# Performance work log

Measured on AMD Instinct MI355X. Metric: run time of the kernel, lower is better.

Reference implementation:

```python
import jax, jax.numpy as jnp
import numpy as np


def setup_inputs() -> dict:
    key = jax.random.key(0)
    ks = jax.random.split(key, 5)
    B, DEC, ENC, H = 4, 256, 256, 512  # feature_dim = hl_size = 512, mlp hidden = 512
    decoder_states = jax.random.normal(ks[0], (B, DEC, H), dtype=jnp.float32)
    encoder_states = jax.random.normal(ks[1], (B, ENC, H), dtype=jnp.float32)
    ext_mask = jnp.zeros((B, DEC, ENC), dtype=bool)  # self.mask set externally; all-False here
    W_mlp = jax.random.normal(ks[2], (2 * H, H), dtype=jnp.float32) * 0.02  # Linear(2H -> H)
    b_mlp = jnp.zeros((H,), dtype=jnp.float32)
    W_out = jax.random.normal(ks[3], (H, 1), dtype=jnp.float32) * 0.02  # Linear(H -> 1)
    b_out = jnp.zeros((1,), dtype=jnp.float32)
    return {"decoder_states": decoder_states, "encoder_states": encoder_states,
            "ext_mask": ext_mask, "W_mlp": W_mlp, "b_mlp": b_mlp,
            "W_out": W_out, "b_out": b_out}


def reference(decoder_states, encoder_states, ext_mask, W_mlp, b_mlp, W_out, b_out):
    # decoder_states: [B, dec, H]; encoder_states: [B, enc, H]
    H = encoder_states.shape[-1]
    # pad mask: positions where encoder feature-0 equals 0.0 -> [B, 1, enc]
    pad_mask = (encoder_states == 0.0)[:, :, :1]
    pad_mask = jnp.swapaxes(pad_mask, 1, 2)  # [B, 1, enc]
    # cat(enc, dec) @ W_mlp  ==  enc @ W_mlp[:H] + dec @ W_mlp[H:]  (avoids 2H concat)
    enc_proj = jnp.einsum('beh,hm->bem', encoder_states, W_mlp[:H])   # [B, enc, Hm]
    dec_proj = jnp.einsum('bdh,hm->bdm', decoder_states, W_mlp[H:])   # [B, dec, Hm]
    hidden = jnp.tanh(dec_proj[:, :, None, :] + enc_proj[:, None, :, :] + b_mlp)  # [B, dec, enc, Hm]
    attn = jnp.einsum('bdem,mo->bde', hidden, W_out) + b_out[0]       # [B, dec, enc]
    attn = jnp.where(ext_mask, -jnp.inf, attn)
    attn = jnp.where(pad_mask, -jnp.inf, attn)
    attn = jax.nn.softmax(attn, axis=-1)
    context = jnp.einsum('bde,beh->bdh', attn, encoder_states)        # [B, dec, H]
    return (context, attn)
```

## Files before the change

### kernel.cpp

```cpp
#include <hip/hip_runtime.h>
#include <math.h>

#define B 4
#define DEC 256
#define ENC 256
#define HDIM 512

#define TANH_SCALE 2.8853900817779268f
#define LOG2E 1.4426950408889634f

__device__ __forceinline__ float fast_exp2(float x) { return __builtin_amdgcn_exp2f(x); }
__device__ __forceinline__ float fast_rcp(float x)  { return __builtin_amdgcn_rcpf(x); }

typedef __attribute__((ext_vector_type(8))) short bf16x8;
typedef __attribute__((ext_vector_type(4))) short bf16x4;
typedef __attribute__((ext_vector_type(4))) float f32x4;
typedef __attribute__((ext_vector_type(4))) unsigned int u32x4;

__device__ __forceinline__ unsigned short bf16_rne(float x) {
    unsigned u = __float_as_uint(x);
    return (unsigned short)((u + 0x7FFFu + ((u >> 16) & 1u)) >> 16);
}
__device__ __forceinline__ float bf16_to_f(unsigned short h) {
    return __uint_as_float((unsigned)h << 16);
}

#define W_OFS(m, k) ((((long)(m) >> 4) << 13) + (((long)(k) >> 3) << 7) + (((m) & 15) << 3) + ((k) & 7))

__global__ __launch_bounds__(256) void convert_kernel(
    const float* __restrict__ enc, const float* __restrict__ dec,
    const float* __restrict__ Wmlp,
    unsigned short* __restrict__ Xh_e, unsigned short* __restrict__ Xl_e,
    unsigned short* __restrict__ Xh_d, unsigned short* __restrict__ Xl_d,
    unsigned short* __restrict__ Wh_e, unsigned short* __restrict__ Wl_e,
    unsigned short* __restrict__ Wh_d, unsigned short* __restrict__ Wl_d,
    unsigned char* __restrict__ padm)
{
    const int tid = threadIdx.x, z = blockIdx.z;
    if (z < 2) {
        const float* X = z ? dec : enc;
        unsigned short* H = z ? Xh_d : Xh_e;
        unsigned short* L = z ? Xl_d : Xl_e;
        const long i8 = ((long)blockIdx.x * 256 + tid) * 8;
        float4 v0 = *(const float4*)(X + i8);
        float4 v1 = *(const float4*)(X + i8 + 4);
        if (z == 0 && (i8 & 511) == 0)
            padm[i8 >> 9] = (v0.x == 0.0f) ? 1 : 0;
        float xs[8] = {v0.x, v0.y, v0.z, v0.w, v1.x, v1.y, v1.z, v1.w};
        bf16x8 hv, lv;
#pragma unroll
        for (int j = 0; j < 8; ++j) {
            unsigned short h = bf16_rne(xs[j]);
            hv[j] = (short)h;
            lv[j] = (short)bf16_rne(xs[j] - bf16_to_f(h));
        }
        *(bf16x8*)(H + i8) = hv;
        *(bf16x8*)(L + i8) = lv;
    } else {
        const float* Wsrc = Wmlp + (z == 3 ? (long)HDIM * HDIM : 0);
        unsigned short* H = (z == 3) ? Wh_d : Wh_e;
        unsigned short* L = (z == 3) ? Wl_d : Wl_e;
        const int t = blockIdx.x * 256 + tid;
        const int m = t & 511;
        const int k0 = (t >> 9) << 2;
        bf16x4 hv, lv;
#pragma unroll
        for (int j = 0; j < 4; ++j) {
            float x = Wsrc[(long)(k0 + j) * 512 + m];
            unsigned short h = bf16_rne(x);
            hv[j] = (short)h;
            lv[j] = (short)bf16_rne(x - bf16_to_f(h));
        }
        const long ofs = W_OFS(m, k0);
        *(bf16x4*)(H + ofs) = hv;
        *(bf16x4*)(L + ofs) = lv;
    }
}

__global__ __launch_bounds__(256) void proj_mfma_kernel(
    const unsigned short* __restrict__ Xh_e, const unsigned short* __restrict__ Xl_e,
    const unsigned short* __restrict__ Xh_d, const unsigned short* __restrict__ Xl_d,
    const unsigned short* __restrict__ Wh_e, const unsigned short* __restrict__ Wl_e,
    const unsigned short* __restrict__ Wh_d, const unsigned short* __restrict__ Wl_d,
    const float* __restrict__ bmlp,
    unsigned int* __restrict__ ET2, float* __restrict__ Dmat)
{
    const int tid = threadIdx.x;
    const int wave = tid >> 6, lane = tid & 63;
    const int z = blockIdx.z;
    const int r0w = blockIdx.x * 64 + wave * 16;
    const int m0 = blockIdx.y * 32;
    const unsigned short* Xh = z ? Xh_d : Xh_e;
    const unsigned short* Xl = z ? Xl_d : Xl_e;
    const unsigned short* Wh = z ? Wh_d : Wh_e;
    const unsigned short* Wl = z ? Wl_d : Wl_e;

    const int col = lane & 15;
    const int quad = lane >> 4;

    const unsigned short* pah = Xh + (long)(r0w + col) * 512 + quad * 8;
    const unsigned short* pal = Xl + (long)(r0w + col) * 512 + quad * 8;
    const long bofs = ((long)(m0 >> 4) << 13) + (quad << 7) + (col << 3);
    const unsigned short* pb0h = Wh + bofs;
    const unsigned short* pb0l = Wl + bofs;
    const unsigned short* pb1h = Wh + bofs + 8192;
    const unsigned short* pb1l = Wl + bofs + 8192;

    f32x4 a0h = {0.f,0.f,0.f,0.f}, a0x = {0.f,0.f,0.f,0.f};
    f32x4 a1h = {0.f,0.f,0.f,0.f}, a1x = {0.f,0.f,0.f,0.f};

    bf16x8 Ah = *(const bf16x8*)pah,  Al = *(const bf16x8*)pal;
    bf16x8 B0h = *(const bf16x8*)pb0h, B0l = *(const bf16x8*)pb0l;
    bf16x8 B1h = *(const bf16x8*)pb1h, B1l = *(const bf16x8*)pb1l;

#pragma unroll 1
    for (int k0 = 0; k0 < 512; k0 += 32) {
        bf16x8 nAh = Ah, nAl = Al, nB0h = B0h, nB0l = B0l, nB1h = B1h, nB1l = B1l;
        if (k0 + 32 < 512) {
            nAh = *(const bf16x8*)(pah + k0 + 32);
            nAl = *(const bf16x8*)(pal + k0 + 32);
            const long ko = (long)(k0 + 32) << 4;
            nB0h = *(const bf16x8*)(pb0h + ko);
            nB0l = *(const bf16x8*)(pb0l + ko);
            nB1h = *(const bf16x8*)(pb1h + ko);
            nB1l = *(const bf16x8*)(pb1l + ko);
        }
        a0h = __builtin_amdgcn_mfma_f32_16x16x32_bf16(Ah, B0h, a0h, 0, 0, 0);
        a1h = __builtin_amdgcn_mfma_f32_16x16x32_bf16(Ah, B1h, a1h, 0, 0, 0);
        a0x = __builtin_amdgcn_mfma_f32_16x16x32_bf16(Ah, B0l, a0x, 0, 0, 0);
        a1x = __builtin_amdgcn_mfma_f32_16x16x32_bf16(Ah, B1l, a1x, 0, 0, 0);
        a0x = __builtin_amdgcn_mfma_f32_16x16x32_bf16(Al, B0h, a0x, 0, 0, 0);
        a1x = __builtin_amdgcn_mfma_f32_16x16x32_bf16(Al, B1h, a1x, 0, 0, 0);
        Ah = nAh; Al = nAl; B0h = nB0h; B0l = nB0l; B1h = nB1h; B1l = nB1l;
    }

    if (z == 0) {
        const int batch = r0w >> 8;
        const int e0 = (r0w & 255) + quad * 4;
        const int p = blockIdx.y * 16 + col;
        u32x4 v;
#pragma unroll
        for (int i = 0; i < 4; ++i) {
            float E0 = fast_exp2((a0h[i] + a0x[i]) * TANH_SCALE);
            float E1 = fast_exp2((a1h[i] + a1x[i]) * TANH_SCALE);
            v[i] = ((unsigned)bf16_rne(E1) << 16) | (unsigned)bf16_rne(E0);
        }
        *(u32x4*)&ET2[(long)batch * 65536 + (long)p * 256 + e0] = v;
    } else {
        const float bq0 = bmlp[m0 + col];
        const float bq1 = bmlp[m0 + 16 + col];
        const int r = r0w + quad * 4;
#pragma unroll
        for (int i = 0; i < 4; ++i) {
            Dmat[(long)(r + i) * HDIM + m0 + col] =
                fast_exp2((a0h[i] + a0x[i] + bq0) * TANH_SCALE);
            Dmat[(long)(r + i) * HDIM + m0 + 16 + col] =
                fast_exp2((a1h[i] + a1x[i] + bq1) * TANH_SCALE);
        }
    }
}

__global__ __launch_bounds__(256) void attn_kernel(
    const float* __restrict__ Dmat, const unsigned int* __restrict__ ET2,
    const float* __restrict__ wo,
    const unsigned char* __restrict__ padm, const unsigned char* __restrict__ extm,
    float* __restrict__ attn_out)
{
    __shared__ __align__(16) float d0s[HDIM];
    __shared__ __align__(16) float d1s[HDIM];
    __shared__ __align__(16) float wos[HDIM];
    __shared__ float red[2][4][2];

    const int tid = threadIdx.x, lane = tid & 63, wave = tid >> 6;
    const int b = blockIdx.y, d0 = blockIdx.x * 2;

    const float* D0 = Dmat + ((long)b * DEC + d0) * HDIM;
    const unsigned int* ecol = ET2 + (long)b * 65536 + tid;

    *(float2*)&d0s[tid * 2] = *(const float2*)&D0[tid * 2];
    *(float2*)&d1s[tid * 2] = *(const float2*)&D0[HDIM + tid * 2];
    *(float2*)&wos[tid * 2] = *(const float2*)&wo[tid * 2];

    unsigned int ev[8], nv[8];
#pragma unroll
    for (int j = 0; j < 8; ++j) ev[j] = ecol[j * 256];
    __syncthreads();

    float acc0 = 0.f, acc1 = 0.f;
    for (int c = 0; c < 256; c += 8) {
        if (c + 8 < 256) {
#pragma unroll
            for (int j = 0; j < 8; ++j) nv[j] = ecol[(c + 8 + j) * 256];
        }
        const int mlb = ((c >> 4) << 5) + (c & 15);
        const int mhb = mlb + 16;
        float4 dv0l[2], dv0h[2], dv1l[2], dv1h[2], wvl[2], wvh[2];
#pragma unroll
        for (int q = 0; q < 2; ++q) {
            dv0l[q] = *(const float4*)&d0s[mlb + q * 4];
            dv0h[q] = *(const float4*)&d0s[mhb + q * 4];
            dv1l[q] = *(const float4*)&d1s[mlb + q * 4];
            dv1h[q] = *(const float4*)&d1s[mhb + q * 4];
            wvl[q]  = *(const float4*)&wos[mlb + q * 4];
            wvh[q]  = *(const float4*)&wos[mhb + q * 4];
        }
#pragma unroll
        for (int j = 0; j < 8; ++j) {
            const float elo = __uint_as_float(ev[j] << 16);
            const float ehi = __uint_as_float(ev[j] & 0xFFFF0000u);
            const float wl = ((const float*)&wvl[j >> 2])[j & 3];
            const float wh = ((const float*)&wvh[j >> 2])[j & 3];
            float t;
            t = fmaf(elo, ((const float*)&dv0l[j >> 2])[j & 3], 1.0f);
            acc0 = fmaf(wl, fast_rcp(t), acc0);
            t = fmaf(ehi, ((const float*)&dv0h[j >> 2])[j & 3], 1.0f);
            acc0 = fmaf(wh, fast_rcp(t), acc0);
            t = fmaf(elo, ((const float*)&dv1l[j >> 2])[j & 3], 1.0f);
            acc1 = fmaf(wl, fast_rcp(t), acc1);
            t = fmaf(ehi, ((const float*)&dv1h[j >> 2])[j & 3], 1.0f);
            acc1 = fmaf(wh, fast_rcp(t), acc1);
        }
#pragma unroll
        for (int j = 0; j < 8; ++j) ev[j] = nv[j];
    }

    const int e = tid;
    const bool pad = (padm[b * ENC + e] != 0);
    const bool x0m = extm[((long)(b * DEC) + d0) * ENC + e] != 0;
    const bool x1m = extm[((long)(b * DEC) + d0 + 1) * ENC + e] != 0;
    float l0 = (pad || x0m) ? -__builtin_inff() : -2.0f * acc0;
    float l1 = (pad || x1m) ? -__builtin_inff() : -2.0f * acc1;

    float m0 = l0, m1 = l1;
#pragma unroll
    for (int off = 32; off >= 1; off >>= 1) {
        m0 = fmaxf(m0, __shfl_xor(m0, off, 64));
        m1 = fmaxf(m1, __shfl_xor(m1, off, 64));
    }
    if (lane == 0) { red[0][wave][0] = m0; red[0][wave][1] = m1; }
    __syncthreads();
    const float gm0 = fmaxf(fmaxf(red[0][0][0], red[0][1][0]), fmaxf(red[0][2][0], red[0][3][0]));
    const float gm1 = fmaxf(fmaxf(red[0][0][1], red[0][1][1]), fmaxf(red[0][2][1], red[0][3][1]));
    float p0 = fast_exp2((l0 - gm0) * LOG2E);
    float p1 = fast_exp2((l1 - gm1) * LOG2E);
    float s0 = p0, s1 = p1;
#pragma unroll
    for (int off = 32; off >= 1; off >>= 1) {
        s0 += __shfl_xor(s0, off, 64);
        s1 += __shfl_xor(s1, off, 64);
    }
    if (lane == 0) { red[1][wave][0] = s0; red[1][wave][1] = s1; }
    __syncthreads();
    const float gs0 = red[1][0][0] + red[1][1][0] + red[1][2][0] + red[1][3][0];
    const float gs1 = red[1][0][1] + red[1][1][1] + red[1][2][1] + red[1][3][1];
    attn_out[((long)(b * DEC) + d0) * ENC + e] = p0 * fast_rcp(gs0);
    attn_out[((long)(b * DEC) + d0 + 1) * ENC + e] = p1 * fast_rcp(gs1);
}

#define C5_LOADW(WB, KOFF)                                                  \
    _Pragma("unroll")                                                       \
    for (int kk = 0; kk < 8; ++kk)                                          \
        WB[kk] = *(const float4*)&We[(long)((KOFF) + kk) * HDIM];

#define C5_FMA(WB, KOFF)                                                    \
    _Pragma("unroll")                                                       \
    for (int q = 0; q < 2; ++q) {                                           \
        float4 xq0 = *(const float4*)&as8[r0l][(KOFF) + q * 4];             \
        float4 xq1 = *(const float4*)&as8[r0l + 1][(KOFF) + q * 4];         \
        _Pragma("unroll")                                                   \
        for (int kk = 0; kk < 4; ++kk) {                                    \
            float4 w = WB[q * 4 + kk];                                      \
            float xv0 = ((const float*)&xq0)[kk];                           \
            float xv1 = ((const float*)&xq1)[kk];                           \
            acc[0][0] = fmaf(xv0, w.x, acc[0][0]);                          \
            acc[0][1] = fmaf(xv0, w.y, acc[0][1]);                          \
            acc[0][2] = fmaf(xv0, w.z, acc[0][2]);                          \
            acc[0][3] = fmaf(xv0, w.w, acc[0][3]);                          \
            acc[1][0] = fmaf(xv1, w.x, acc[1][0]);                          \
            acc[1][1] = fmaf(xv1, w.y, acc[1][1]);                          \
            acc[1][2] = fmaf(xv1, w.z, acc[1][2]);                          \
            acc[1][3] = fmaf(xv1, w.w, acc[1][3]);                          \
        }                                                                   \
    }

__global__ __launch_bounds__(256) void context_kernel(
    const float* __restrict__ attn, const float* __restrict__ enc,
    float* __restrict__ ctx)
{
    __shared__ __align__(16) float as8[8][ENC];
    const int tid = threadIdx.x;
    const int tx = tid & 63, ty = tid >> 6;
    const int r0 = blockIdx.x * 8;
    const int b = r0 >> 8;
    const int h0 = blockIdx.y * 256 + tx * 4;
    const int r0l = ty * 2;
    const float* We = enc + (long)b * ENC * HDIM + h0;

    {
        const float* ag = attn + (long)r0 * ENC;
#pragma unroll
        for (int i = 0; i < 2; ++i) {
            int idx = (tid + i * 256) * 4;
            *(float4*)&as8[0][idx] = *(const float4*)&ag[idx];
        }
    }

    float acc[2][4] = {};
    float4 Wa[8], Wb[8];
    C5_LOADW(Wa, 0)
    __syncthreads();

    for (int k0 = 0; k0 < ENC; k0 += 16) {
        C5_LOADW(Wb, k0 + 8)
        C5_FMA(Wa, k0)
        if (k0 + 16 < ENC) { C5_LOADW(Wa, k0 + 16) }
        C5_FMA(Wb, k0 + 8)
    }

#pragma unroll
    for (int i = 0; i < 2; ++i)
        *(float4*)&ctx[(long)(r0 + r0l + i) * HDIM + h0] =
            make_float4(acc[i][0], acc[i][1], acc[i][2], acc[i][3]);
}

extern "C" void kernel_launch(void* const* d_in, const int* in_sizes, int n_in,
                              void* d_out, int out_size, void* d_ws, size_t ws_size,
                              hipStream_t stream) {
    const float* dec = (const float*)d_in[0];
    const float* enc = (const float*)d_in[1];
    const unsigned char* extm = (const unsigned char*)d_in[2];
    const float* Wmlp = (const float*)d_in[3];
    const float* bmlp = (const float*)d_in[4];
    const float* Wout = (const float*)d_in[5];

    float* ctx = (float*)d_out;
    float* attn = ctx + (size_t)B * DEC * HDIM;

    const size_t F = (size_t)B * DEC * HDIM;
    unsigned int* ET2 = (unsigned int*)d_ws;
    float* Dmat = (float*)(ET2 + (size_t)B * 65536);
    unsigned short* Xh_e = (unsigned short*)(Dmat + F);
    unsigned short* Xl_e = Xh_e + F;
    unsigned short* Xh_d = Xl_e + F;
    unsigned short* Xl_d = Xh_d + F;
    unsigned short* Wh_e = Xl_d + F;
    unsigned short* Wl_e = Wh_e + HDIM * HDIM;
    unsigned short* Wh_d = Wl_e + HDIM * HDIM;
    unsigned short* Wl_d = Wh_d + HDIM * HDIM;
    unsigned char* padm = (unsigned char*)(Wl_d + HDIM * HDIM);

    convert_kernel<<<dim3(256, 1, 4), 256, 0, stream>>>(
        enc, dec, Wmlp, Xh_e, Xl_e, Xh_d, Xl_d, Wh_e, Wl_e, Wh_d, Wl_d, padm);
    proj_mfma_kernel<<<dim3(16, 16, 2), 256, 0, stream>>>(
        Xh_e, Xl_e, Xh_d, Xl_d, Wh_e, Wl_e, Wh_d, Wl_d, bmlp, ET2, Dmat);
    attn_kernel<<<dim3(DEC / 2, B), 256, 0, stream>>>(Dmat, ET2, Wout, padm, extm, attn);
    context_kernel<<<dim3(128, 2), 256, 0, stream>>>(attn, enc, ctx);
}
```

Measured before the change: 121.3 us.

## Fuse four kernels into one cooperative persistent kernel with grid syncs

Replaces the convert, projection, attention-score and context launches with a single cooperative kernel of 512 blocks that runs each stage in turn, separated by grid-wide barriers. The aim is to cut per-launch overhead and the tail bubbles between kernels. The context stage is remapped to one output row per wave to fit the fixed grid. The cost is grid-sync latency, a launch bound that caps register use to allow 2 blocks per CU, and some stages now run with a different block count than before.

```diff
diff --git a/kernel.cpp b/kernel.cpp
--- a/kernel.cpp
+++ b/kernel.cpp
@@ -1,5 +1,8 @@
 #include <hip/hip_runtime.h>
+#include <hip/hip_cooperative_groups.h>
 #include <math.h>
+
+namespace cg = cooperative_groups;
 
 #define B 4
 #define DEC 256
@@ -27,332 +30,312 @@
 
 #define W_OFS(m, k) ((((long)(m) >> 4) << 13) + (((long)(k) >> 3) << 7) + (((m) & 15) << 3) + ((k) & 7))
 
-__global__ __launch_bounds__(256) void convert_kernel(
-    const float* __restrict__ enc, const float* __restrict__ dec,
-    const float* __restrict__ Wmlp,
-    unsigned short* __restrict__ Xh_e, unsigned short* __restrict__ Xl_e,
-    unsigned short* __restrict__ Xh_d, unsigned short* __restrict__ Xl_d,
-    unsigned short* __restrict__ Wh_e, unsigned short* __restrict__ Wl_e,
-    unsigned short* __restrict__ Wh_d, unsigned short* __restrict__ Wl_d,
-    unsigned char* __restrict__ padm)
+struct KArgs {
+    const float* dec; const float* enc; const float* Wmlp; const float* bmlp; const float* wo;
+    const unsigned char* extm;
+    float* ctx; float* attn;
+    unsigned short *Xh_e, *Xl_e, *Xh_d, *Xl_d, *Wh_e, *Wl_e, *Wh_d, *Wl_d;
+    unsigned int* ET2; float* Dmat; unsigned char* padm;
+};
+
+__global__ __launch_bounds__(256, 2) void fused_kernel(KArgs a)
 {
-    const int tid = threadIdx.x, z = blockIdx.z;
-    if (z < 2) {
-        const float* X = z ? dec : enc;
-        unsigned short* H = z ? Xh_d : Xh_e;
-        unsigned short* L = z ? Xl_d : Xl_e;
-        const long i8 = ((long)blockIdx.x * 256 + tid) * 8;
-        float4 v0 = *(const float4*)(X + i8);
-        float4 v1 = *(const float4*)(X + i8 + 4);
-        if (z == 0 && (i8 & 511) == 0)
-            padm[i8 >> 9] = (v0.x == 0.0f) ? 1 : 0;
-        float xs[8] = {v0.x, v0.y, v0.z, v0.w, v1.x, v1.y, v1.z, v1.w};
-        bf16x8 hv, lv;
-#pragma unroll
-        for (int j = 0; j < 8; ++j) {
-            unsigned short h = bf16_rne(xs[j]);
-            hv[j] = (short)h;
-            lv[j] = (short)bf16_rne(xs[j] - bf16_to_f(h));
-        }
-        *(bf16x8*)(H + i8) = hv;
-        *(bf16x8*)(L + i8) = lv;
-    } else {
-        const float* Wsrc = Wmlp + (z == 3 ? (long)HDIM * HDIM : 0);
-        unsigned short* H = (z == 3) ? Wh_d : Wh_e;
-        unsigned short* L = (z == 3) ? Wl_d : Wl_e;
-        const int t = blockIdx.x * 256 + tid;
-        const int m = t & 511;
-        const int k0 = (t >> 9) << 2;
-        bf16x4 hv, lv;
-#pragma unroll
-        for (int j = 0; j < 4; ++j) {
-            float x = Wsrc[(long)(k0 + j) * 512 + m];
-            unsigned short h = bf16_rne(x);
-            hv[j] = (short)h;
-            lv[j] = (short)bf16_rne(x - bf16_to_f(h));
-        }
-        const long ofs = W_OFS(m, k0);
-        *(bf16x4*)(H + ofs) = hv;
-        *(bf16x4*)(L + ofs) = lv;
+    cg::grid_group gridg = cg::this_grid();
+    __shared__ __align__(16) char smem[8192];
+    const int tid = threadIdx.x;
+    const int bid = blockIdx.x;
+
+    for (int u = bid; u < 1024; u += 512) {
+        const int z = u >> 8, bx = u & 255;
+        if (z < 2) {
+            const float* X = z ? a.dec : a.enc;
+            unsigned short* H = z ? a.Xh_d : a.Xh_e;
+            unsigned short* L = z ? a.Xl_d : a.Xl_e;
+            const long i8 = ((long)bx * 256 + tid) * 8;
+            float4 v0 = *(const float4*)(X + i8);
+            float4 v1 = *(const float4*)(X + i8 + 4);
+            if (z == 0 && (i8 & 511) == 0)
+                a.padm[i8 >> 9] = (v0.x == 0.0f) ? 1 : 0;
+            float xs[8] = {v0.x, v0.y, v0.z, v0.w, v1.x, v1.y, v1.z, v1.w};
+            bf16x8 hv, lv;
+#pragma unroll
+            for (int j = 0; j < 8; ++j) {
+                unsigned short h = bf16_rne(xs[j]);
+                hv[j] = (short)h;
+                lv[j] = (short)bf16_rne(xs[j] - bf16_to_f(h));
+            }
+            *(bf16x8*)(H + i8) = hv;
+            *(bf16x8*)(L + i8) = lv;
+        } else {
+            const float* Wsrc = a.Wmlp + (z == 3 ? (long)HDIM * HDIM : 0);
+            unsigned short* H = (z == 3) ? a.Wh_d : a.Wh_e;
+            unsigned short* L = (z == 3) ? a.Wl_d : a.Wl_e;
+            const int t = bx * 256 + tid;
+            const int m = t & 511;
+            const int k0 = (t >> 9) << 2;
+            bf16x4 hv, lv;
+#pragma unroll
+            for (int j = 0; j < 4; ++j) {
+                float x = Wsrc[(long)(k0 + j) * 512 + m];
+                unsigned short h = bf16_rne(x);
+                hv[j] = (short)h;
+                lv[j] = (short)bf16_rne(x - bf16_to_f(h));
+            }
+            const long ofs = W_OFS(m, k0);
+            *(bf16x4*)(H + ofs) = hv;
+            *(bf16x4*)(L + ofs) = lv;
+        }
     }
-}
-
-__global__ __launch_bounds__(256) void proj_mfma_kernel(
-    const unsigned short* __restrict__ Xh_e, const unsigned short* __restrict__ Xl_e,
-    const unsigned short* __restrict__ Xh_d, const unsigned short* __restrict__ Xl_d,
-    const unsigned short* __restrict__ Wh_e, const unsigned short* __restrict__ Wl_e,
-    const unsigned short* __restrict__ Wh_d, const unsigned short* __restrict__ Wl_d,
-    const float* __restrict__ bmlp,
-    unsigned int* __restrict__ ET2, float* __restrict__ Dmat)
-{
-    const int tid = threadIdx.x;
-    const int wave = tid >> 6, lane = tid & 63;
-    const int z = blockIdx.z;
-    const int r0w = blockIdx.x * 64 + wave * 16;
-    const int m0 = blockIdx.y * 32;
-    const unsigned short* Xh = z ? Xh_d : Xh_e;
-    const unsigned short* Xl = z ? Xl_d : Xl_e;
-    const unsigned short* Wh = z ? Wh_d : Wh_e;
-    const unsigned short* Wl = z ? Wl_d : Wl_e;
-
-    const int col = lane & 15;
-    const int quad = lane >> 4;
-
-    const unsigned short* pah = Xh + (long)(r0w + col) * 512 + quad * 8;
-    const unsigned short* pal = Xl + (long)(r0w + col) * 512 + quad * 8;
-    const long bofs = ((long)(m0 >> 4) << 13) + (quad << 7) + (col << 3);
-    const unsigned short* pb0h = Wh + bofs;
-    const unsigned short* pb0l = Wl + bofs;
-    const unsigned short* pb1h = Wh + bofs + 8192;
-    const unsigned short* pb1l = Wl + bofs + 8192;
-
-    f32x4 a0h = {0.f,0.f,0.f,0.f}, a0x = {0.f,0.f,0.f,0.f};
-    f32x4 a1h = {0.f,0.f,0.f,0.f}, a1x = {0.f,0.f,0.f,0.f};
-
-    bf16x8 Ah = *(const bf16x8*)pah,  Al = *(const bf16x8*)pal;
-    bf16x8 B0h = *(const bf16x8*)pb0h, B0l = *(const bf16x8*)pb0l;
-    bf16x8 B1h = *(const bf16x8*)pb1h, B1l = *(const bf16x8*)pb1l;
+    gridg.sync();
+
+    {
+        const int wave = tid >> 6, lane = tid & 63;
+        const int z = bid >> 8;
+        const int r0w = (bid & 15) * 64 + wave * 16;
+        const int m0 = ((bid >> 4) & 15) * 32;
+        const unsigned short* Xh = z ? a.Xh_d : a.Xh_e;
+        const unsigned short* Xl = z ? a.Xl_d : a.Xl_e;
+        const unsigned short* Wh = z ? a.Wh_d : a.Wh_e;
+        const unsigned short* Wl = z ? a.Wl_d : a.Wl_e;
+
+        const int col = lane & 15;
+        const int quad = lane >> 4;
+
+        const unsigned short* pah = Xh + (long)(r0w + col) * 512 + quad * 8;
+        const unsigned short* pal = Xl + (long)(r0w + col) * 512 + quad * 8;
+        const long bofs = ((long)(m0 >> 4) << 13) + (quad << 7) + (col << 3);
+        const unsigned short* pb0h = Wh + bofs;
+        const unsigned short* pb0l = Wl + bofs;
+        const unsigned short* pb1h = Wh + bofs + 8192;
+        const unsigned short* pb1l = Wl + bofs + 8192;
+
+        f32x4 a0h = {0.f,0.f,0.f,0.f}, a0x = {0.f,0.f,0.f,0.f};
+        f32x4 a1h = {0.f,0.f,0.f,0.f}, a1x = {0.f,0.f,0.f,0.f};
+
+        bf16x8 Ah = *(const bf16x8*)pah,  Al = *(const bf16x8*)pal;
+        bf16x8 B0h = *(const bf16x8*)pb0h, B0l = *(const bf16x8*)pb0l;
+        bf16x8 B1h = *(const bf16x8*)pb1h, B1l = *(const bf16x8*)pb1l;
 
 #pragma unroll 1
-    for (int k0 = 0; k0 < 512; k0 += 32) {
-        bf16x8 nAh = Ah, nAl = Al, nB0h = B0h, nB0l = B0l, nB1h = B1h, nB1l = B1l;
-        if (k0 + 32 < 512) {
-            nAh = *(const bf16x8*)(pah + k0 + 32);
-            nAl = *(const bf16x8*)(pal + k0 + 32);
-            const long ko = (long)(k0 + 32) << 4;
-            nB0h = *(const bf16x8*)(pb0h + ko);
-            nB0l = *(const bf16x8*)(pb0l + ko);
-            nB1h = *(const bf16x8*)(pb1h + ko);
-            nB1l = *(const bf16x8*)(pb1l + ko);
-        }
-        a0h = __builtin_amdgcn_mfma_f32_16x16x32_bf16(Ah, B0h, a0h, 0, 0, 0);
-        a1h = __builtin_amdgcn_mfma_f32_16x16x32_bf16(Ah, B1h, a1h, 0, 0, 0);
-        a0x = __builtin_amdgcn_mfma_f32_16x16x32_bf16(Ah, B0l, a0x, 0, 0, 0);
-        a1x = __builtin_amdgcn_mfma_f32_16x16x32_bf16(Ah, B1l, a1x, 0, 0, 0);
-        a0x = __builtin_amdgcn_mfma_f32_16x16x32_bf16(Al, B0h, a0x, 0, 0, 0);
-        a1x = __builtin_amdgcn_mfma_f32_16x16x32_bf16(Al, B1h, a1x, 0, 0, 0);
-        Ah = nAh; Al = nAl; B0h = nB0h; B0l = nB0l; B1h = nB1h; B1l = nB1l;
+        for (int k0 = 0; k0 < 512; k0 += 32) {
+            bf16x8 nAh = Ah, nAl = Al, nB0h = B0h, nB0l = B0l, nB1h = B1h, nB1l = B1l;
+            if (k0 + 32 < 512) {
+                nAh = *(const bf16x8*)(pah + k0 + 32);
+                nAl = *(const bf16x8*)(pal + k0 + 32);
+                const long ko = (long)(k0 + 32) << 4;
+                nB0h = *(const bf16x8*)(pb0h + ko);
+                nB0l = *(const bf16x8*)(pb0l + ko);
+                nB1h = *(const bf16x8*)(pb1h + ko);
+                nB1l = *(const bf16x8*)(pb1l + ko);
+            }
+            a0h = __builtin_amdgcn_mfma_f32_16x16x32_bf16(Ah, B0h, a0h, 0, 0, 0);
+            a1h = __builtin_amdgcn_mfma_f32_16x16x32_bf16(Ah, B1h, a1h, 0, 0, 0);
+            a0x = __builtin_amdgcn_mfma_f32_16x16x32_bf16(Ah, B0l, a0x, 0, 0, 0);
+            a1x = __builtin_amdgcn_mfma_f32_16x16x32_bf16(Ah, B1l, a1x, 0, 0, 0);
+            a0x = __builtin_amdgcn_mfma_f32_16x16x32_bf16(Al, B0h, a0x, 0, 0, 0);
+            a1x = __builtin_amdgcn_mfma_f32_16x16x32_bf16(Al, B1h, a1x, 0, 0, 0);
+            Ah = nAh; Al = nAl; B0h = nB0h; B0l = nB0l; B1h = nB1h; B1l = nB1l;
+        }
+
+        if (z == 0) {
+            const int batch = r0w >> 8;
+            const int e0 = (r0w & 255) + quad * 4;
+            const int p = ((bid >> 4) & 15) * 16 + col;
+            u32x4 v;
+#pragma unroll
+            for (int i = 0; i < 4; ++i) {
+                float E0 = fast_exp2((a0h[i] + a0x[i]) * TANH_SCALE);
+                float E1 = fast_exp2((a1h[i] + a1x[i]) * TANH_SCALE);
+                v[i] = ((unsigned)bf16_rne(E1) << 16) | (unsigned)bf16_rne(E0);
+            }
+            *(u32x4*)&a.ET2[(long)batch * 65536 + (long)p * 256 + e0] = v;
+        } else {
+            const float bq0 = a.bmlp[m0 + col];
+            const float bq1 = a.bmlp[m0 + 16 + col];
+            const int r = r0w + quad * 4;
+#pragma unroll
+            for (int i = 0; i < 4; ++i) {
+                a.Dmat[(long)(r + i) * HDIM + m0 + col] =
+                    fast_exp2((a0h[i] + a0x[i] + bq0) * TANH_SCALE);
+                a.Dmat[(long)(r + i) * HDIM + m0 + 16 + col] =
+                    fast_exp2((a1h[i] + a1x[i] + bq1) * TANH_SCALE);
+            }
+        }
     }
-
-    if (z == 0) {
-        const int batch = r0w >> 8;
-        const int e0 = (r0w & 255) + quad * 4;
-        const int p = blockIdx.y * 16 + col;
-        u32x4 v;
-#pragma unroll
-        for (int i = 0; i < 4; ++i) {
-            float E0 = fast_exp2((a0h[i] + a0x[i]) * TANH_SCALE);
-            float E1 = fast_exp2((a1h[i] + a1x[i]) * TANH_SCALE);
-            v[i] = ((unsigned)bf16_rne(E1) << 16) | (unsigned)bf16_rne(E0);
-        }
-        *(u32x4*)&ET2[(long)batch * 65536 + (long)p * 256 + e0] = v;
-    } else {
-        const float bq0 = bmlp[m0 + col];
-        const float bq1 = bmlp[m0 + 16 + col];
-        const int r = r0w + quad * 4;
-#pragma unroll
-        for (int i = 0; i < 4; ++i) {
-            Dmat[(long)(r + i) * HDIM + m0 + col] =
-                fast_exp2((a0h[i] + a0x[i] + bq0) * TANH_SCALE);
-            Dmat[(long)(r + i) * HDIM + m0 + 16 + col] =
-                fast_exp2((a1h[i] + a1x[i] + bq1) * TANH_SCALE);
-        }
+    gridg.sync();
+
+    {
+        float* d0s = (float*)smem;
+        float* d1s = d0s + 512;
+        float* wos = d1s + 512;
+        float (*red)[4][2] = (float(*)[4][2])(wos + 512);
+
+        const int lane = tid & 63, wave = tid >> 6;
+        const int b = bid >> 7, d0 = (bid & 127) * 2;
+
+        const float* D0 = a.Dmat + ((long)b * DEC + d0) * HDIM;
+        const unsigned int* ecol = a.ET2 + (long)b * 65536 + tid;
+
+        *(float2*)&d0s[tid * 2] = *(const float2*)&D0[tid * 2];
+        *(float2*)&d1s[tid * 2] = *(const float2*)&D0[HDIM + tid * 2];
+        *(float2*)&wos[tid * 2] = *(const float2*)&a.wo[tid * 2];
+
+        unsigned int ev[8], nv[8];
+#pragma unroll
+        for (int j = 0; j < 8; ++j) ev[j] = ecol[j * 256];
+        __syncthreads();
+
+        float acc0 = 0.f, acc1 = 0.f;
+        for (int c = 0; c < 256; c += 8) {
+            if (c + 8 < 256) {
+#pragma unroll
+                for (int j = 0; j < 8; ++j) nv[j] = ecol[(c + 8 + j) * 256];
+            }
+            const int mlb = ((c >> 4) << 5) + (c & 15);
+            const int mhb = mlb + 16;
+            float4 dv0l[2], dv0h[2], dv1l[2], dv1h[2], wvl[2], wvh[2];
+#pragma unroll
+            for (int q = 0; q < 2; ++q) {
+                dv0l[q] = *(const float4*)&d0s[mlb + q * 4];
+                dv0h[q] = *(const float4*)&d0s[mhb + q * 4];
+                dv1l[q] = *(const float4*)&d1s[mlb + q * 4];
+                dv1h[q] = *(const float4*)&d1s[mhb + q * 4];
+                wvl[q]  = *(const float4*)&wos[mlb + q * 4];
+                wvh[q]  = *(const float4*)&wos[mhb + q * 4];
+            }
+#pragma unroll
+            for (int j = 0; j < 8; ++j) {
+                const float elo = __uint_as_float(ev[j] << 16);
+                const float ehi = __uint_as_float(ev[j] & 0xFFFF0000u);
+                const float wl = ((const float*)&wvl[j >> 2])[j & 3];
+                const float wh = ((const float*)&wvh[j >> 2])[j & 3];
+                float t;
+                t = fmaf(elo, ((const float*)&dv0l[j >> 2])[j & 3], 1.0f);
+                acc0 = fmaf(wl, fast_rcp(t), acc0);
+                t = fmaf(ehi, ((const float*)&dv0h[j >> 2])[j & 3], 1.0f);
+                acc0 = fmaf(wh, fast_rcp(t), acc0);
+                t = fmaf(elo, ((const float*)&dv1l[j >> 2])[j & 3], 1.0f);
+                acc1 = fmaf(wl, fast_rcp(t), acc1);
+                t = fmaf(ehi, ((const float*)&dv1h[j >> 2])[j & 3], 1.0f);
+                acc1 = fmaf(wh, fast_rcp(t), acc1);
+            }
+#pragma unroll
+            for (int j = 0; j < 8; ++j) ev[j] = nv[j];
+        }
+
+        const int e = tid;
+        const bool pad = (a.padm[b * ENC + e] != 0);
+        const bool x0m = a.extm[((long)(b * DEC) + d0) * ENC + e] != 0;
+        const bool x1m = a.extm[((long)(b * DEC) + d0 + 1) * ENC + e] != 0;
+        float l0 = (pad || x0m) ? -__builtin_inff() : -2.0f * acc0;
+        float l1 = (pad || x1m) ? -__builtin_inff() : -2.0f * acc1;
+
+        float m0 = l0, m1 = l1;
+#pragma unroll
+        for (int off = 32; off >= 1; off >>= 1) {
+            m0 = fmaxf(m0, __shfl_xor(m0, off, 64));
+            m1 = fmaxf(m1, __shfl_xor(m1, off, 64));
+        }
+        if (lane == 0) { red[0][wave][0] = m0; red[0][wave][1] = m1; }
+        __syncthreads();
+        const float gm0 = fmaxf(fmaxf(red[0][0][0], red[0][1][0]), fmaxf(red[0][2][0], red[0][3][0]));
+        const float gm1 = fmaxf(fmaxf(red[0][0][1], red[0][1][1]), fmaxf(red[0][2][1], red[0][3][1]));
+        float p0 = fast_exp2((l0 - gm0) * LOG2E);
+        float p1 = fast_exp2((l1 - gm1) * LOG2E);
+        float s0 = p0, s1 = p1;
+#pragma unroll
+        for (int off = 32; off >= 1; off >>= 1) {
+            s0 += __shfl_xor(s0, off, 64);
+            s1 += __shfl_xor(s1, off, 64);
+        }
+        if (lane == 0) { red[1][wave][0] = s0; red[1][wave][1] = s1; }
+        __syncthreads();
+        const float gs0 = red[1][0][0] + red[1][1][0] + red[1][2][0] + red[1][3][0];
+        const float gs1 = red[1][0][1] + red[1][1][1] + red[1][2][1] + red[1][3][1];
+        a.attn[((long)(b * DEC) + d0) * ENC + e] = p0 * fast_rcp(gs0);
+        a.attn[((long)(b * DEC) + d0 + 1) * ENC + e] = p1 * fast_rcp(gs1);
     }
-}
-
-__global__ __launch_bounds__(256) void attn_kernel(
-    const float* __restrict__ Dmat, const unsigned int* __restrict__ ET2,
-    const float* __restrict__ wo,
-    const unsigned char* __restrict__ padm, const unsigned char* __restrict__ extm,
-    float* __restrict__ attn_out)
-{
-    __shared__ __align__(16) float d0s[HDIM];
-    __shared__ __align__(16) float d1s[HDIM];
-    __shared__ __align__(16) float wos[HDIM];
-    __shared__ float red[2][4][2];
-
-    const int tid = threadIdx.x, lane = tid & 63, wave = tid >> 6;
-    const int b = blockIdx.y, d0 = blockIdx.x * 2;
-
-    const float* D0 = Dmat + ((long)b * DEC + d0) * HDIM;
-    const unsigned int* ecol = ET2 + (long)b * 65536 + tid;
-
-    *(float2*)&d0s[tid * 2] = *(const float2*)&D0[tid * 2];
-    *(float2*)&d1s[tid * 2] = *(const float2*)&D0[HDIM + tid * 2];
-    *(float2*)&wos[tid * 2] = *(const float2*)&wo[tid * 2];
-
-    unsigned int ev[8], nv[8];
-#pragma unroll
-    for (int j = 0; j < 8; ++j) ev[j] = ecol[j * 256];
-    __syncthreads();
-
-    float acc0 = 0.f, acc1 = 0.f;
-    for (int c = 0; c < 256; c += 8) {
-        if (c + 8 < 256) {
-#pragma unroll
-            for (int j = 0; j < 8; ++j) nv[j] = ecol[(c + 8 + j) * 256];
-        }
-        const int mlb = ((c >> 4) << 5) + (c & 15);
-        const int mhb = mlb + 16;
-        float4 dv0l[2], dv0h[2], dv1l[2], dv1h[2], wvl[2], wvh[2];
-#pragma unroll
-        for (int q = 0; q < 2; ++q) {
-            dv0l[q] = *(const float4*)&d0s[mlb + q * 4];
-            dv0h[q] = *(const float4*)&d0s[mhb + q * 4];
-            dv1l[q] = *(const float4*)&d1s[mlb + q * 4];
-            dv1h[q] = *(const float4*)&d1s[mhb + q * 4];
-            wvl[q]  = *(const float4*)&wos[mlb + q * 4];
-            wvh[q]  = *(const float4*)&wos[mhb + q * 4];
-        }
-#pragma unroll
-        for (int j = 0; j < 8; ++j) {
-            const float elo = __uint_as_float(ev[j] << 16);
-            const float ehi = __uint_as_float(ev[j] & 0xFFFF0000u);
-            const float wl = ((const float*)&wvl[j >> 2])[j & 3];
-            const float wh = ((const float*)&wvh[j >> 2])[j & 3];
-            float t;
-            t = fmaf(elo, ((const float*)&dv0l[j >> 2])[j & 3], 1.0f);
-            acc0 = fmaf(wl, fast_rcp(t), acc0);
-            t = fmaf(ehi, ((const float*)&dv0h[j >> 2])[j & 3], 1.0f);
-            acc0 = fmaf(wh, fast_rcp(t), acc0);
-            t = fmaf(elo, ((const float*)&dv1l[j >> 2])[j & 3], 1.0f);
-            acc1 = fmaf(wl, fast_rcp(t), acc1);
-            t = fmaf(ehi, ((const float*)&dv1h[j >> 2])[j & 3], 1.0f);
-            acc1 = fmaf(wh, fast_rcp(t), acc1);
-        }
-#pragma unroll
-        for (int j = 0; j < 8; ++j) ev[j] = nv[j];
+    gridg.sync();
+
+    {
+        float* as8 = (float*)smem;
+        const int rg = bid & 127, hs = bid >> 7;
+        const int r0 = rg * 8;
+        const int bb = r0 >> 8;
+        const int tx = tid & 31, ty = tid >> 5;
+        const int h0 = hs * 128 + tx * 4;
+        const float* We = a.enc + (long)bb * ENC * HDIM + h0;
+        const float* ag = a.attn + (long)r0 * ENC;
+
+        *(float4*)&as8[tid * 4] = *(const float4*)&ag[tid * 4];
+        *(float4*)&as8[(tid + 256) * 4] = *(const float4*)&ag[(tid + 256) * 4];
+
+        float4 Wa[8], Wb[8];
+#pragma unroll
+        for (int kk = 0; kk < 8; ++kk) Wa[kk] = *(const float4*)&We[(long)kk * HDIM];
+        __syncthreads();
+
+        float ac0 = 0.f, ac1 = 0.f, ac2 = 0.f, ac3 = 0.f;
+        for (int e0 = 0; e0 < 256; e0 += 16) {
+#pragma unroll
+            for (int kk = 0; kk < 8; ++kk)
+                Wb[kk] = *(const float4*)&We[(long)(e0 + 8 + kk) * HDIM];
+#pragma unroll
+            for (int kk = 0; kk < 8; ++kk) {
+                float av = as8[ty * 256 + e0 + kk];
+                float4 w = Wa[kk];
+                ac0 = fmaf(av, w.x, ac0);
+                ac1 = fmaf(av, w.y, ac1);
+                ac2 = fmaf(av, w.z, ac2);
+                ac3 = fmaf(av, w.w, ac3);
+            }
+            if (e0 + 16 < 256) {
+#pragma unroll
+                for (int kk = 0; kk < 8; ++kk)
+                    Wa[kk] = *(const float4*)&We[(long)(e0 + 16 + kk) * HDIM];
+            }
+#pragma unroll
+            for (int kk = 0; kk < 8; ++kk) {
+                float av = as8[ty * 256 + e0 + 8 + kk];
+                float4 w = Wb[kk];
+                ac0 = fmaf(av, w.x, ac0);
+                ac1 = fmaf(av, w.y, ac1);
+                ac2 = fmaf(av, w.z, ac2);
+                ac3 = fmaf(av, w.w, ac3);
+            }
+        }
+        *(float4*)&a.ctx[(long)(r0 + ty) * HDIM + h0] = make_float4(ac0, ac1, ac2, ac3);
     }
-
-    const int e = tid;
-    const bool pad = (padm[b * ENC + e] != 0);
-    const bool x0m = extm[((long)(b * DEC) + d0) * ENC + e] != 0;
-    const bool x1m = extm[((long)(b * DEC) + d0 + 1) * ENC + e] != 0;
-    float l0 = (pad || x0m) ? -__builtin_inff() : -2.0f * acc0;
-    float l1 = (pad || x1m) ? -__builtin_inff() : -2.0f * acc1;
-
-    float m0 = l0, m1 = l1;
-#pragma unroll
-    for (int off = 32; off >= 1; off >>= 1) {
-        m0 = fmaxf(m0, __shfl_xor(m0, off, 64));
-        m1 = fmaxf(m1, __shfl_xor(m1, off, 64));
-    }
-    if (lane == 0) { red[0][wave][0] = m0; red[0][wave][1] = m1; }
-    __syncthreads();
-    const float gm0 = fmaxf(fmaxf(red[0][0][0], red[0][1][0]), fmaxf(red[0][2][0], red[0][3][0]));
-    const float gm1 = fmaxf(fmaxf(red[0][0][1], red[0][1][1]), fmaxf(red[0][2][1], red[0][3][1]));
-    float p0 = fast_exp2((l0 - gm0) * LOG2E);
-    float p1 = fast_exp2((l1 - gm1) * LOG2E);
-    float s0 = p0, s1 = p1;
-#pragma unroll
-    for (int off = 32; off >= 1; off >>= 1) {
-        s0 += __shfl_xor(s0, off, 64);
-        s1 += __shfl_xor(s1, off, 64);
-    }
-    if (lane == 0) { red[1][wave][0] = s0; red[1][wave][1] = s1; }
-    __syncthreads();
-    const float gs0 = red[1][0][0] + red[1][1][0] + red[1][2][0] + red[1][3][0];
-    const float gs1 = red[1][0][1] + red[1][1][1] + red[1][2][1] + red[1][3][1];
-    attn_out[((long)(b * DEC) + d0) * ENC + e] = p0 * fast_rcp(gs0);
-    attn_out[((long)(b * DEC) + d0 + 1) * ENC + e] = p1 * fast_rcp(gs1);
-}
-
-#define C5_LOADW(WB, KOFF)                                                  \
-    _Pragma("unroll")                                                       \
-    for (int kk = 0; kk < 8; ++kk)                                          \
-        WB[kk] = *(const float4*)&We[(long)((KOFF) + kk) * HDIM];
-
-#define C5_FMA(WB, KOFF)                                                    \
-    _Pragma("unroll")                                                       \
-    for (int q = 0; q < 2; ++q) {                                           \
-        float4 xq0 = *(const float4*)&as8[r0l][(KOFF) + q * 4];             \
-        float4 xq1 = *(const float4*)&as8[r0l + 1][(KOFF) + q * 4];         \
-        _Pragma("unroll")                                                   \
-        for (int kk = 0; kk < 4; ++kk) {                                    \
-            float4 w = WB[q * 4 + kk];                                      \
-            float xv0 = ((const float*)&xq0)[kk];                           \
-            float xv1 = ((const float*)&xq1)[kk];                           \
-            acc[0][0] = fmaf(xv0, w.x, acc[0][0]);                          \
-            acc[0][1] = fmaf(xv0, w.y, acc[0][1]);                          \
-            acc[0][2] = fmaf(xv0, w.z, acc[0][2]);                          \
-            acc[0][3] = fmaf(xv0, w.w, acc[0][3]);                          \
-            acc[1][0] = fmaf(xv1, w.x, acc[1][0]);                          \
-            acc[1][1] = fmaf(xv1, w.y, acc[1][1]);                          \
-            acc[1][2] = fmaf(xv1, w.z, acc[1][2]);                          \
-            acc[1][3] = fmaf(xv1, w.w, acc[1][3]);                          \
-        }                                                                   \
-    }
-
-__global__ __launch_bounds__(256) void context_kernel(
-    const float* __restrict__ attn, const float* __restrict__ enc,
-    float* __restrict__ ctx)
-{
-    __shared__ __align__(16) float as8[8][ENC];
-    const int tid = threadIdx.x;
-    const int tx = tid & 63, ty = tid >> 6;
-    const int r0 = blockIdx.x * 8;
-    const int b = r0 >> 8;
-    const int h0 = blockIdx.y * 256 + tx * 4;
-    const int r0l = ty * 2;
-    const float* We = enc + (long)b * ENC * HDIM + h0;
-
-    {
-        const float* ag = attn + (long)r0 * ENC;
-#pragma unroll
-        for (int i = 0; i < 2; ++i) {
-            int idx = (tid + i * 256) * 4;
-            *(float4*)&as8[0][idx] = *(const float4*)&ag[idx];
-        }
-    }
-
-    float acc[2][4] = {};
-    float4 Wa[8], Wb[8];
-    C5_LOADW(Wa, 0)
-    __syncthreads();
-
-    for (int k0 = 0; k0 < ENC; k0 += 16) {
-        C5_LOADW(Wb, k0 + 8)
-        C5_FMA(Wa, k0)
-        if (k0 + 16 < ENC) { C5_LOADW(Wa, k0 + 16) }
-        C5_FMA(Wb, k0 + 8)
-    }
-
-#pragma unroll
-    for (int i = 0; i < 2; ++i)
-        *(float4*)&ctx[(long)(r0 + r0l + i) * HDIM + h0] =
-            make_float4(acc[i][0], acc[i][1], acc[i][2], acc[i][3]);
 }
 
 extern "C" void kernel_launch(void* const* d_in, const int* in_sizes, int n_in,
                               void* d_out, int out_size, void* d_ws, size_t ws_size,
                               hipStream_t stream) {
-    const float* dec = (const float*)d_in[0];
-    const float* enc = (const float*)d_in[1];
-    const unsigned char* extm = (const unsigned char*)d_in[2];
-    const float* Wmlp = (const float*)d_in[3];
-    const float* bmlp = (const float*)d_in[4];
-    const float* Wout = (const float*)d_in[5];
-
-    float* ctx = (float*)d_out;
-    float* attn = ctx + (size_t)B * DEC * HDIM;
+    KArgs ha;
+    ha.dec  = (const float*)d_in[0];
+    ha.enc  = (const float*)d_in[1];
+    ha.extm = (const unsigned char*)d_in[2];
+    ha.Wmlp = (const float*)d_in[3];
+    ha.bmlp = (const float*)d_in[4];
+    ha.wo   = (const float*)d_in[5];
+
+    ha.ctx  = (float*)d_out;
+    ha.attn = ha.ctx + (size_t)B * DEC * HDIM;
 
     const size_t F = (size_t)B * DEC * HDIM;
-    unsigned int* ET2 = (unsigned int*)d_ws;
-    float* Dmat = (float*)(ET2 + (size_t)B * 65536);
-    unsigned short* Xh_e = (unsigned short*)(Dmat + F);
-    unsigned short* Xl_e = Xh_e + F;
-    unsigned short* Xh_d = Xl_e + F;
-    unsigned short* Xl_d = Xh_d + F;
-    unsigned short* Wh_e = Xl_d + F;
-    unsigned short* Wl_e = Wh_e + HDIM * HDIM;
-    unsigned short* Wh_d = Wl_e + HDIM * HDIM;
-    unsigned short* Wl_d = Wh_d + HDIM * HDIM;
-    unsigned char* padm = (unsigned char*)(Wl_d + HDIM * HDIM);
-
-    convert_kernel<<<dim3(256, 1, 4), 256, 0, stream>>>(
-        enc, dec, Wmlp, Xh_e, Xl_e, Xh_d, Xl_d, Wh_e, Wl_e, Wh_d, Wl_d, padm);
-    proj_mfma_kernel<<<dim3(16, 16, 2), 256, 0, stream>>>(
-        Xh_e, Xl_e, Xh_d, Xl_d, Wh_e, Wl_e, Wh_d, Wl_d, bmlp, ET2, Dmat);
-    attn_kernel<<<dim3(DEC / 2, B), 256, 0, stream>>>(Dmat, ET2, Wout, padm, extm, attn);
-    context_kernel<<<dim3(128, 2), 256, 0, stream>>>(attn, enc, ctx);
+    ha.ET2  = (unsigned int*)d_ws;
+    ha.Dmat = (float*)(ha.ET2 + (size_t)B * 65536);
+    ha.Xh_e = (unsigned short*)(ha.Dmat + F);
+    ha.Xl_e = ha.Xh_e + F;
+    ha.Xh_d = ha.Xl_e + F;
+    ha.Xl_d = ha.Xh_d + F;
+    ha.Wh_e = ha.Xl_d + F;
+    ha.Wl_e = ha.Wh_e + HDIM * HDIM;
+    ha.Wh_d = ha.Wl_e + HDIM * HDIM;
+    ha.Wl_d = ha.Wh_d + HDIM * HDIM;
+    ha.padm = (unsigned char*)(ha.Wl_d + HDIM * HDIM);
+
+    void* params[] = { (void*)&ha };
+    hipLaunchCooperativeKernel((void*)fused_kernel, dim3(512), dim3(256),
+                               params, 0, stream);
 }
```

New measurement: 314.8 us. +159.4%, slower.
